# Optimization experiments

Measured on AMD Instinct MI355X. Metric: run time of the kernel, lower is better.

## Reference

```python
import jax, jax.numpy as jnp
import numpy as np
import math

D_MODEL = 512
NHEAD = 8
HEAD = D_MODEL // NHEAD


def _pe(length, d):
    pos = np.arange(length)[:, None].astype(np.float32)
    div = np.exp(np.arange(0, d, 2).astype(np.float32) * (-math.log(10000.0) / d))
    pe = np.zeros((length, d), np.float32)
    pe[:, 0::2] = np.sin(pos * div)
    pe[:, 1::2] = np.cos(pos * div)
    return jnp.asarray(pe)


def _ln(x, g, b, eps=1e-5):
    m = x.mean(-1, keepdims=True)
    v = ((x - m) ** 2).mean(-1, keepdims=True)
    return (x - m) / jnp.sqrt(v + eps) * g + b


def _mha(q_in, k_in, v_in, w_in, b_in, w_out, b_out, mask=None):
    d = q_in.shape[-1]
    wq, wk, wv = jnp.split(w_in, 3, axis=0)
    bq, bk, bv = jnp.split(b_in, 3, axis=0)
    B, Sq, _ = q_in.shape
    Sk = k_in.shape[1]
    q = (q_in @ wq.T + bq).reshape(B, Sq, NHEAD, HEAD)
    k = (k_in @ wk.T + bk).reshape(B, Sk, NHEAD, HEAD)
    v = (v_in @ wv.T + bv).reshape(B, Sk, NHEAD, HEAD)
    s = jnp.einsum('bqhd,bkhd->bhqk', q, k) / math.sqrt(HEAD)
    if mask is not None:
        s = s + mask
    a = jax.nn.softmax(s, axis=-1)
    o = jnp.einsum('bhqk,bkhd->bqhd', a, v).reshape(B, Sq, d)
    return o @ w_out.T + b_out


def setup_inputs() -> dict:
    rng = np.random.default_rng(0)
    def r(*s):
        return jnp.asarray(rng.standard_normal(s, dtype=np.float32) * 0.02)
    L, d, ff, di, do = 6, 512, 2048, 64, 64
    B, S, T = 4, 512, 256
    return dict(
        src=jnp.asarray(rng.standard_normal((B, S, di), dtype=np.float32)),
        tgt=jnp.asarray(rng.standard_normal((B, T, do), dtype=np.float32)),
        enc_in_w=r(d, di), enc_in_b=r(d),
        dec_in_w=r(d, do), dec_in_b=r(d),
        out_w=r(do, d), out_b=r(do),
        enc_attn_w=r(L, 3 * d, d), enc_attn_b=r(L, 3 * d),
        enc_out_w=r(L, d, d), enc_out_b=r(L, d),
        enc_ff1_w=r(L, ff, d), enc_ff1_b=r(L, ff),
        enc_ff2_w=r(L, d, ff), enc_ff2_b=r(L, d),
        enc_ln1_g=jnp.ones((L, d)), enc_ln1_b=jnp.zeros((L, d)),
        enc_ln2_g=jnp.ones((L, d)), enc_ln2_b=jnp.zeros((L, d)),
        dec_sa_w=r(L, 3 * d, d), dec_sa_b=r(L, 3 * d),
        dec_sa_out_w=r(L, d, d), dec_sa_out_b=r(L, d),
        dec_ca_w=r(L, 3 * d, d), dec_ca_b=r(L, 3 * d),
        dec_ca_out_w=r(L, d, d), dec_ca_out_b=r(L, d),
        dec_ff1_w=r(L, ff, d), dec_ff1_b=r(L, ff),
        dec_ff2_w=r(L, d, ff), dec_ff2_b=r(L, d),
        dec_ln1_g=jnp.ones((L, d)), dec_ln1_b=jnp.zeros((L, d)),
        dec_ln2_g=jnp.ones((L, d)), dec_ln2_b=jnp.zeros((L, d)),
        dec_ln3_g=jnp.ones((L, d)), dec_ln3_b=jnp.zeros((L, d)),
    )


def reference(src, tgt, enc_in_w, enc_in_b, dec_in_w, dec_in_b, out_w, out_b,
              enc_attn_w, enc_attn_b, enc_out_w, enc_out_b,
              enc_ff1_w, enc_ff1_b, enc_ff2_w, enc_ff2_b,
              enc_ln1_g, enc_ln1_b, enc_ln2_g, enc_ln2_b,
              dec_sa_w, dec_sa_b, dec_sa_out_w, dec_sa_out_b,
              dec_ca_w, dec_ca_b, dec_ca_out_w, dec_ca_out_b,
              dec_ff1_w, dec_ff1_b, dec_ff2_w, dec_ff2_b,
              dec_ln1_g, dec_ln1_b, dec_ln2_g, dec_ln2_b, dec_ln3_g, dec_ln3_b):
    d = D_MODEL
    sq = math.sqrt(d)
    S, T = src.shape[1], tgt.shape[1]
    L = enc_attn_w.shape[0]
    # encoder: 'cosine' pos encoding (dropout disabled / eval)
    x = (src @ enc_in_w.T + enc_in_b) * sq + _pe(S, d)[None]
    for i in range(L):
        a = _mha(x, x, x, enc_attn_w[i], enc_attn_b[i], enc_out_w[i], enc_out_b[i])
        x = _ln(x + a, enc_ln1_g[i], enc_ln1_b[i])
        f = jax.nn.relu(x @ enc_ff1_w[i].T + enc_ff1_b[i]) @ enc_ff2_w[i].T + enc_ff2_b[i]
        x = _ln(x + f, enc_ln2_g[i], enc_ln2_b[i])
    memory = x
    # decoder: teacher-forced prefix loop == single causal-masked pass.
    # NOTE: original adds pe[0] to EVERY step (pos_encoder on a length-1 slice).
    y = (tgt @ dec_in_w.T + dec_in_b) * sq + _pe(1, d)[0]
    mask = jnp.where(jnp.tril(jnp.ones((T, T), bool)), 0.0, -1e9).astype(y.dtype)
    for i in range(L):
        a = _mha(y, y, y, dec_sa_w[i], dec_sa_b[i], dec_sa_out_w[i], dec_sa_out_b[i], mask)
        y = _ln(y + a, dec_ln1_g[i], dec_ln1_b[i])
        c = _mha(y, memory, memory, dec_ca_w[i], dec_ca_b[i], dec_ca_out_w[i], dec_ca_out_b[i])
        y = _ln(y + c, dec_ln2_g[i], dec_ln2_b[i])
        f = jax.nn.relu(y @ dec_ff1_w[i].T + dec_ff1_b[i]) @ dec_ff2_w[i].T + dec_ff2_b[i]
        y = _ln(y + f, dec_ln3_g[i], dec_ln3_b[i])
    return y @ out_w.T + out_b
```

## Files before the change

### kernel.cpp

```cpp
#include <hip/hip_runtime.h>
#include <hip/hip_bf16.h>
#include <math.h>

#define BB 4
#define SEQ 512
#define TGT 256
#define DM 512
#define FFD 2048
#define NH 8
#define HD 64
#define NL 6

typedef unsigned short u16;
typedef __attribute__((ext_vector_type(4))) float f4;
typedef __attribute__((ext_vector_type(4))) unsigned short us4;
typedef __attribute__((ext_vector_type(8))) unsigned short us8;
typedef __attribute__((ext_vector_type(8))) short s8;

__device__ inline u16 f2b(float f) {
    __hip_bfloat16 h = __float2bfloat16(f);
    return *reinterpret_cast<u16*>(&h);
}
__device__ inline float b2f(u16 u) {
    unsigned int x = ((unsigned int)u) << 16;
    float f;
    __builtin_memcpy(&f, &x, 4);
    return f;
}
__device__ inline us4 cvt4(f4 v) {
    us4 u;
    u.x = f2b(v.x); u.y = f2b(v.y); u.z = f2b(v.z); u.w = f2b(v.w);
    return u;
}

struct CastSegs {
    const float* src[24];
    u16* dst[24];
    int cum[25];
    int nseg;
};

__global__ __launch_bounds__(256) void castseg_k(CastSegs cs)
{
    int i = blockIdx.x * blockDim.x + threadIdx.x;
    if (i >= cs.cum[cs.nseg]) return;
    int s = 0;
    while (i >= cs.cum[s + 1]) s++;
    int local = i - cs.cum[s];
    const f4* sp = (const f4*)cs.src[s] + (size_t)local * 2;
    f4 lo = sp[0], hi = sp[1];
    us4 ul = cvt4(lo), uh = cvt4(hi);
    us8 o;
#pragma unroll
    for (int e = 0; e < 4; e++) { o[e] = ul[e]; o[e + 4] = uh[e]; }
    ((us8*)cs.dst[s])[local] = o;
}

__global__ void kvbias_k(const float* __restrict__ dec_ca_b, float* __restrict__ out)
{
    int idx = blockIdx.x * blockDim.x + threadIdx.x;
    if (idx >= NL * 2 * DM) return;
    int layer = idx >> 10, j = idx & 1023;
    out[idx] = dec_ca_b[layer * 3 * DM + DM + j];
}

template <int RELU, int OUTF32, int BM, int PE>
__global__ __launch_bounds__(256) void mgemm_k(
    const u16* __restrict__ A, const u16* __restrict__ W,
    const float* __restrict__ bias, const u16* __restrict__ resid,
    void* __restrict__ Cv, int M, int N, int K, float alpha)
{
    constexpr int MI = BM / 32;
    __shared__ u16 As[2][BM][72];
    __shared__ u16 Bs[2][64][72];
    const int bm = blockIdx.y * BM, bn = blockIdx.x * 64;
    const int tid = threadIdx.x;
    const int wave = tid >> 6, lane = tid & 63;
    const int wr = (wave >> 1) * (BM / 2), wc = (wave & 1) * 32;
    const int lm = lane & 15, quad = lane >> 4;
    const int sbr = tid >> 2, sbc = (tid & 3) * 16;
    const int sar = (BM == 64) ? (tid >> 2) : (tid >> 3);
    const int sac = (BM == 64) ? ((tid & 3) * 16) : ((tid & 7) * 8);

    const u16* Arow = A + (size_t)(bm + sar) * K + sac;
    const u16* Wrow = W + (size_t)(bn + sbr) * K + sbc;

    us8 a0 = *(const us8*)(Arow);
    us8 a1;
    if (BM == 64) a1 = *(const us8*)(Arow + 8);
    us8 b0 = *(const us8*)(Wrow);
    us8 b1 = *(const us8*)(Wrow + 8);

    f4 acc[MI][2];
#pragma unroll
    for (int i = 0; i < MI; i++)
#pragma unroll
        for (int j = 0; j < 2; j++) acc[i][j] = (f4)(0.f);

    const int nk = K >> 6;
    *(us8*)&As[0][sar][sac] = a0;
    if (BM == 64) *(us8*)&As[0][sar][sac + 8] = a1;
    *(us8*)&Bs[0][sbr][sbc] = b0;
    *(us8*)&Bs[0][sbr][sbc + 8] = b1;
    __syncthreads();

    for (int t = 0; t < nk; t++) {
        const int cb = t & 1;
        if (t + 1 < nk) {
            int off = (t + 1) << 6;
            a0 = *(const us8*)(Arow + off);
            if (BM == 64) a1 = *(const us8*)(Arow + off + 8);
            b0 = *(const us8*)(Wrow + off);
            b1 = *(const us8*)(Wrow + off + 8);
        }
#pragma unroll
        for (int ks = 0; ks < 2; ks++) {
            s8 af[MI], bfr[2];
#pragma unroll
            for (int i = 0; i < MI; i++) af[i] = *(const s8*)&As[cb][wr + i * 16 + lm][ks * 32 + quad * 8];
#pragma unroll
            for (int j = 0; j < 2; j++) bfr[j] = *(const s8*)&Bs[cb][wc + j * 16 + lm][ks * 32 + quad * 8];
#pragma unroll
            for (int i = 0; i < MI; i++)
#pragma unroll
                for (int j = 0; j < 2; j++)
                    acc[i][j] = __builtin_amdgcn_mfma_f32_16x16x32_bf16(af[i], bfr[j], acc[i][j], 0, 0, 0);
        }
        if (t + 1 < nk) {
            const int nb = cb ^ 1;
            *(us8*)&As[nb][sar][sac] = a0;
            if (BM == 64) *(us8*)&As[nb][sar][sac + 8] = a1;
            *(us8*)&Bs[nb][sbr][sbc] = b0;
            *(us8*)&Bs[nb][sbr][sbc + 8] = b1;
            __syncthreads();
        }
    }

#pragma unroll
    for (int j = 0; j < 2; j++) {
        int n = bn + wc + j * 16 + lm;
        float bv = bias[n];
        float dv = 0.f;
        if (PE == 1) dv = expf((float)(n & ~1) * (-9.210340371976184f / (float)DM));
#pragma unroll
        for (int i = 0; i < MI; i++) {
#pragma unroll
            for (int r = 0; r < 4; r++) {
                int m = bm + wr + i * 16 + quad * 4 + r;
                float v = (acc[i][j][r] + bv) * alpha;
                if (PE == 1) {
                    float ang = (float)(m & (SEQ - 1)) * dv;
                    v += (n & 1) ? cosf(ang) : sinf(ang);
                }
                if (PE == 2) { if (n & 1) v += 1.f; }
                if (RELU) v = fmaxf(v, 0.f);
                size_t off = (size_t)m * N + n;
                if (resid) v += b2f(resid[off]);
                if (OUTF32) ((float*)Cv)[off] = v;
                else        ((u16*)Cv)[off]  = f2b(v);
            }
        }
    }
}

template <int RELU>
__global__ __launch_bounds__(256) void mgemm128_k(
    const u16* __restrict__ A, const u16* __restrict__ W,
    const float* __restrict__ bias, u16* __restrict__ C,
    int M, int N, int K)
{
    __shared__ u16 As[2][64][72];
    __shared__ u16 Bs[2][128][72];
    const int bm = blockIdx.y * 64, bn = blockIdx.x * 128;
    const int tid = threadIdx.x;
    const int wave = tid >> 6, lane = tid & 63;
    const int wr = (wave >> 1) * 32, wc = (wave & 1) * 64;
    const int lm = lane & 15, quad = lane >> 4;
    const int sar = tid >> 2, sac = (tid & 3) * 16;
    const int sbr = tid >> 1, sbc = (tid & 1) * 32;

    const u16* Arow = A + (size_t)(bm + sar) * K + sac;
    const u16* Wrow = W + (size_t)(bn + sbr) * K + sbc;

    us8 a0 = *(const us8*)(Arow);
    us8 a1 = *(const us8*)(Arow + 8);
    us8 b0 = *(const us8*)(Wrow);
    us8 b1 = *(const us8*)(Wrow + 8);
    us8 b2 = *(const us8*)(Wrow + 16);
    us8 b3 = *(const us8*)(Wrow + 24);

    f4 acc[2][4];
#pragma unroll
    for (int i = 0; i < 2; i++)
#pragma unroll
        for (int j = 0; j < 4; j++) acc[i][j] = (f4)(0.f);

    const int nk = K >> 6;
    *(us8*)&As[0][sar][sac]     = a0;
    *(us8*)&As[0][sar][sac + 8] = a1;
    *(us8*)&Bs[0][sbr][sbc]      = b0;
    *(us8*)&Bs[0][sbr][sbc + 8]  = b1;
    *(us8*)&Bs[0][sbr][sbc + 16] = b2;
    *(us8*)&Bs[0][sbr][sbc + 24] = b3;
    __syncthreads();

    for (int t = 0; t < nk; t++) {
        const int cb = t & 1;
        if (t + 1 < nk) {
            int off = (t + 1) << 6;
            a0 = *(const us8*)(Arow + off);
            a1 = *(const us8*)(Arow + off + 8);
            b0 = *(const us8*)(Wrow + off);
            b1 = *(const us8*)(Wrow + off + 8);
            b2 = *(const us8*)(Wrow + off + 16);
            b3 = *(const us8*)(Wrow + off + 24);
        }
#pragma unroll
        for (int ks = 0; ks < 2; ks++) {
            s8 af[2], bfr[4];
#pragma unroll
            for (int i = 0; i < 2; i++) af[i] = *(const s8*)&As[cb][wr + i * 16 + lm][ks * 32 + quad * 8];
#pragma unroll
            for (int j = 0; j < 4; j++) bfr[j] = *(const s8*)&Bs[cb][wc + j * 16 + lm][ks * 32 + quad * 8];
#pragma unroll
            for (int i = 0; i < 2; i++)
#pragma unroll
                for (int j = 0; j < 4; j++)
                    acc[i][j] = __builtin_amdgcn_mfma_f32_16x16x32_bf16(af[i], bfr[j], acc[i][j], 0, 0, 0);
        }
        if (t + 1 < nk) {
            const int nb = cb ^ 1;
            *(us8*)&As[nb][sar][sac]     = a0;
            *(us8*)&As[nb][sar][sac + 8] = a1;
            *(us8*)&Bs[nb][sbr][sbc]      = b0;
            *(us8*)&Bs[nb][sbr][sbc + 8]  = b1;
            *(us8*)&Bs[nb][sbr][sbc + 16] = b2;
            *(us8*)&Bs[nb][sbr][sbc + 24] = b3;
            __syncthreads();
        }
    }

#pragma unroll
    for (int j = 0; j < 4; j++) {
        int n = bn + wc + j * 16 + lm;
        float bv = bias[n];
#pragma unroll
        for (int i = 0; i < 2; i++) {
#pragma unroll
            for (int r = 0; r < 4; r++) {
                int m = bm + wr + i * 16 + quad * 4 + r;
                float v = acc[i][j][r] + bv;
                if (RELU) v = fmaxf(v, 0.f);
                C[(size_t)m * N + n] = f2b(v);
            }
        }
    }
}

template <int CAUSAL>
__global__ __launch_bounds__(256) void flash_k(
    const u16* __restrict__ Q, int qs,
    const u16* __restrict__ Kp, int ks,
    const u16* __restrict__ V, int vs,
    u16* __restrict__ O, int Sq, int Sk)
{
    __shared__ u16 Qs[64][72];
    __shared__ u16 Ks[128][72];
    __shared__ u16 Vs[64][136];
    __shared__ u16 Ps[4][16][136];
    const int bm = blockIdx.x * 64;
    const int bh = blockIdx.y, b = bh >> 3, h = bh & 7;
    const int tid = threadIdx.x;
    const int wave = tid >> 6, lane = tid & 63;
    const int lm = lane & 15, quad = lane >> 4;

    const u16* Qb = Q + (size_t)(b * Sq + bm) * qs + h * HD;
    {
        int r = tid >> 2, c = (tid & 3) * 16;
        *(us8*)&Qs[r][c]     = *(const us8*)(Qb + (size_t)r * qs + c);
        *(us8*)&Qs[r][c + 8] = *(const us8*)(Qb + (size_t)r * qs + c + 8);
    }

    float mrow[4], lrow[4];
    f4 o[4];
#pragma unroll
    for (int r = 0; r < 4; r++) { mrow[r] = -1e30f; lrow[r] = 0.f; }
#pragma unroll
    for (int nt = 0; nt < 4; nt++) o[nt] = (f4)(0.f);

    const u16* Kb = Kp + (size_t)(b * Sk) * ks + h * HD;
    const u16* Vb = V + (size_t)(b * Sk) * vs + h * HD;
    int nkt = Sk >> 7;
    if (CAUSAL) { int lim = (bm + 63) / 128 + 1; if (lim < nkt) nkt = lim; }

    const int vd = tid & 63, vkb = tid >> 6;
    const int kr = tid >> 3, kc8 = (tid & 7) * 8;

    for (int kt = 0; kt < nkt; kt++) {
        const u16* Kt = Kb + ((size_t)kt << 7) * ks;
        const u16* Vt = Vb + ((size_t)kt << 7) * vs;
#pragma unroll
        for (int p = 0; p < 4; p++) {
            int r = p * 32 + kr;
            *(us8*)&Ks[r][kc8] = *(const us8*)(Kt + (size_t)r * ks + kc8);
        }
#pragma unroll
        for (int p = 0; p < 32; p++) {
            int kv = p * 4 + vkb;
            Vs[vd][kv] = Vt[(size_t)kv * vs + vd];
        }
        __syncthreads();

        f4 sa[8];
#pragma unroll
        for (int nt = 0; nt < 8; nt++) sa[nt] = (f4)(0.f);
#pragma unroll
        for (int ks2 = 0; ks2 < 2; ks2++) {
            s8 aq = *(const s8*)&Qs[wave * 16 + lm][ks2 * 32 + quad * 8];
#pragma unroll
            for (int nt = 0; nt < 8; nt++) {
                s8 bk = *(const s8*)&Ks[nt * 16 + lm][ks2 * 32 + quad * 8];
                sa[nt] = __builtin_amdgcn_mfma_f32_16x16x32_bf16(aq, bk, sa[nt], 0, 0, 0);
            }
        }
        float tmx[4] = {-1e30f, -1e30f, -1e30f, -1e30f};
#pragma unroll
        for (int nt = 0; nt < 8; nt++) {
#pragma unroll
            for (int r = 0; r < 4; r++) {
                float v = sa[nt][r] * 0.125f;
                if (CAUSAL) {
                    int col = (kt << 7) + nt * 16 + lm;
                    int row = bm + wave * 16 + quad * 4 + r;
                    if (col > row) v = -1e30f;
                }
                sa[nt][r] = v;
                tmx[r] = fmaxf(tmx[r], v);
            }
        }
#pragma unroll
        for (int st = 1; st < 16; st <<= 1)
#pragma unroll
            for (int r = 0; r < 4; r++) tmx[r] = fmaxf(tmx[r], __shfl_xor(tmx[r], st));
        float al[4];
#pragma unroll
        for (int r = 0; r < 4; r++) {
            float mn = fmaxf(mrow[r], tmx[r]);
            al[r] = __expf(mrow[r] - mn);
            mrow[r] = mn;
        }
        float ts[4] = {0.f, 0.f, 0.f, 0.f};
#pragma unroll
        for (int nt = 0; nt < 8; nt++) {
#pragma unroll
            for (int r = 0; r < 4; r++) {
                float pe = __expf(sa[nt][r] - mrow[r]);
                sa[nt][r] = pe;
                ts[r] += pe;
            }
        }
#pragma unroll
        for (int st = 1; st < 16; st <<= 1)
#pragma unroll
            for (int r = 0; r < 4; r++) ts[r] += __shfl_xor(ts[r], st);
#pragma unroll
        for (int r = 0; r < 4; r++) lrow[r] = lrow[r] * al[r] + ts[r];
#pragma unroll
        for (int nt = 0; nt < 4; nt++)
#pragma unroll
            for (int r = 0; r < 4; r++) o[nt][r] *= al[r];
#pragma unroll
        for (int nt = 0; nt < 8; nt++)
#pragma unroll
            for (int r = 0; r < 4; r++)
                Ps[wave][quad * 4 + r][nt * 16 + lm] = f2b(sa[nt][r]);
#pragma unroll
        for (int kc = 0; kc < 4; kc++) {
            s8 ap = *(const s8*)&Ps[wave][lm][kc * 32 + quad * 8];
#pragma unroll
            for (int nt = 0; nt < 4; nt++) {
                s8 bv = *(const s8*)&Vs[nt * 16 + lm][kc * 32 + quad * 8];
                o[nt] = __builtin_amdgcn_mfma_f32_16x16x32_bf16(ap, bv, o[nt], 0, 0, 0);
            }
        }
        __syncthreads();
    }

    float inv[4];
#pragma unroll
    for (int r = 0; r < 4; r++) inv[r] = 1.f / lrow[r];
#pragma unroll
    for (int nt = 0; nt < 4; nt++) {
#pragma unroll
        for (int r = 0; r < 4; r++) {
            int m = bm + wave * 16 + quad * 4 + r;
            O[(size_t)(b * Sq + m) * DM + h * HD + nt * 16 + lm] = f2b(o[nt][r] * inv[r]);
        }
    }
}

__global__ __launch_bounds__(256) void ln_k(u16* __restrict__ x,
                                            const float* __restrict__ g,
                                            const float* __restrict__ b)
{
    const int wave = threadIdx.x >> 6, lane = threadIdx.x & 63;
    const int row = blockIdx.x * 4 + wave;
    u16* xr = x + (size_t)row * DM + lane * 8;
    us8 v8 = *(const us8*)xr;
    float v[8];
    float s = 0.f;
#pragma unroll
    for (int e = 0; e < 8; e++) { v[e] = b2f(v8[e]); s += v[e]; }
#pragma unroll
    for (int st = 1; st < 64; st <<= 1) s += __shfl_xor(s, st);
    float mean = s * (1.f / DM);
    float q = 0.f;
#pragma unroll
    for (int e = 0; e < 8; e++) { float d = v[e] - mean; q += d * d; }
#pragma unroll
    for (int st = 1; st < 64; st <<= 1) q += __shfl_xor(q, st);
    float rstd = rsqrtf(q * (1.f / DM) + 1e-5f);
    f4 g0 = *(const f4*)(g + lane * 8), g1 = *(const f4*)(g + lane * 8 + 4);
    f4 b0 = *(const f4*)(b + lane * 8), b1 = *(const f4*)(b + lane * 8 + 4);
    us8 o;
#pragma unroll
    for (int e = 0; e < 4; e++) {
        o[e]     = f2b((v[e]     - mean) * rstd * g0[e] + b0[e]);
        o[e + 4] = f2b((v[e + 4] - mean) * rstd * g1[e] + b1[e]);
    }
    *(us8*)xr = o;
}

static inline dim3 mg64(int M, int N) { return dim3(N / 64, M / 64); }
static inline dim3 mg32(int M, int N) { return dim3(N / 64, M / 32); }
static inline dim3 mg128(int M, int N) { return dim3(N / 128, M / 64); }

extern "C" void kernel_launch(void* const* d_in, const int* in_sizes, int n_in,
                              void* d_out, int out_size, void* d_ws, size_t ws_size,
                              hipStream_t stream)
{
    const float* src       = (const float*)d_in[0];
    const float* tgt       = (const float*)d_in[1];
    const float* enc_in_w  = (const float*)d_in[2];
    const float* enc_in_b  = (const float*)d_in[3];
    const float* dec_in_w  = (const float*)d_in[4];
    const float* dec_in_b  = (const float*)d_in[5];
    const float* out_w     = (const float*)d_in[6];
    const float* out_b     = (const float*)d_in[7];
    const float* enc_attn_w = (const float*)d_in[8];
    const float* enc_attn_b = (const float*)d_in[9];
    const float* enc_out_w  = (const float*)d_in[10];
    const float* enc_out_b  = (const float*)d_in[11];
    const float* enc_ff1_w  = (const float*)d_in[12];
    const float* enc_ff1_b  = (const float*)d_in[13];
    const float* enc_ff2_w  = (const float*)d_in[14];
    const float* enc_ff2_b  = (const float*)d_in[15];
    const float* enc_ln1_g  = (const float*)d_in[16];
    const float* enc_ln1_b  = (const float*)d_in[17];
    const float* enc_ln2_g  = (const float*)d_in[18];
    const float* enc_ln2_b  = (const float*)d_in[19];
    const float* dec_sa_w     = (const float*)d_in[20];
    const float* dec_sa_b     = (const float*)d_in[21];
    const float* dec_sa_out_w = (const float*)d_in[22];
    const float* dec_sa_out_b = (const float*)d_in[23];
    const float* dec_ca_w     = (const float*)d_in[24];
    const float* dec_ca_b     = (const float*)d_in[25];
    const float* dec_ca_out_w = (const float*)d_in[26];
    const float* dec_ca_out_b = (const float*)d_in[27];
    const float* dec_ff1_w    = (const float*)d_in[28];
    const float* dec_ff1_b    = (const float*)d_in[29];
    const float* dec_ff2_w    = (const float*)d_in[30];
    const float* dec_ff2_b    = (const float*)d_in[31];
    const float* dec_ln1_g    = (const float*)d_in[32];
    const float* dec_ln1_b    = (const float*)d_in[33];
    const float* dec_ln2_g    = (const float*)d_in[34];
    const float* dec_ln2_b    = (const float*)d_in[35];
    const float* dec_ln3_g    = (const float*)d_in[36];
    const float* dec_ln3_b    = (const float*)d_in[37];

    const int ME = BB * SEQ;
    const int MD = BB * TGT;
    const int BH = BB * NH;
    const float SQD = 22.627416997969522f;

    const size_t SZ_ATTN = (size_t)NL * 3 * DM * DM;
    const size_t SZ_OUT  = (size_t)NL * DM * DM;
    const size_t SZ_FF   = (size_t)NL * FFD * DM;

    float* fp = (float*)d_ws;
    float* kvbias = fp; fp += NL * 2 * DM;
    u16* p = (u16*)fp;
    u16* xa   = p; p += (size_t)ME * DM;
    u16* xb   = p; p += (size_t)ME * DM;
    u16* reg1 = p; p += (size_t)ME * FFD;
    u16* tbuf = p; p += (size_t)ME * DM;
    u16* ya   = p; p += (size_t)MD * DM;
    u16* yb   = p; p += (size_t)MD * DM;
    u16* kvall = p; p += (size_t)ME * NL * 2 * DM;
    u16* src_b     = p; p += (size_t)ME * HD;
    u16* tgt_b     = p; p += (size_t)MD * HD;
    u16* enc_in_wb = p; p += (size_t)DM * HD;
    u16* dec_in_wb = p; p += (size_t)DM * HD;
    u16* out_wb    = p; p += (size_t)HD * DM;
    u16* enc_at_wb = p; p += SZ_ATTN;
    u16* enc_ow_wb = p; p += SZ_OUT;
    u16* enc_f1_wb = p; p += SZ_FF;
    u16* enc_f2_wb = p; p += SZ_FF;
    u16* dec_sa_wb = p; p += SZ_ATTN;
    u16* dec_sao_wb = p; p += SZ_OUT;
    u16* dec_ca_wb = p; p += SZ_ATTN;
    u16* dec_cao_wb = p; p += SZ_OUT;
    u16* dec_f1_wb = p; p += SZ_FF;
    u16* dec_f2_wb = p; p += SZ_FF;
    u16* kvstack   = p; p += (size_t)NL * 2 * DM * DM;

    CastSegs cs;
    int ns = 0;
    auto seg = [&](const float* s, u16* d, size_t n) {
        cs.src[ns] = s; cs.dst[ns] = d;
        cs.cum[ns + 1] = cs.cum[ns] + (int)(n / 8);
        ns++;
    };
    cs.cum[0] = 0;
    seg(src,          src_b,     (size_t)ME * HD);
    seg(tgt,          tgt_b,     (size_t)MD * HD);
    seg(enc_in_w,     enc_in_wb, (size_t)DM * HD);
    seg(dec_in_w,     dec_in_wb, (size_t)DM * HD);
    seg(out_w,        out_wb,    (size_t)HD * DM);
    seg(enc_attn_w,   enc_at_wb, SZ_ATTN);
    seg(enc_out_w,    enc_ow_wb, SZ_OUT);
    seg(enc_ff1_w,    enc_f1_wb, SZ_FF);
    seg(enc_ff2_w,    enc_f2_wb, SZ_FF);
    seg(dec_sa_w,     dec_sa_wb, SZ_ATTN);
    seg(dec_sa_out_w, dec_sao_wb, SZ_OUT);
    seg(dec_ca_w,     dec_ca_wb, SZ_ATTN);
    seg(dec_ca_out_w, dec_cao_wb, SZ_OUT);
    seg(dec_ff1_w,    dec_f1_wb, SZ_FF);
    seg(dec_ff2_w,    dec_f2_wb, SZ_FF);
    for (int i = 0; i < NL; i++)
        seg(dec_ca_w + (size_t)i * 3 * DM * DM + (size_t)DM * DM,
            kvstack + (size_t)i * 2 * DM * DM, (size_t)2 * DM * DM);
    cs.nseg = ns;
    castseg_k<<<(cs.cum[ns] + 255) / 256, 256, 0, stream>>>(cs);
    kvbias_k<<<(NL * 2 * DM + 255) / 256, 256, 0, stream>>>(dec_ca_b, kvbias);

    mgemm_k<0, 0, 64, 1><<<mg64(ME, DM), 256, 0, stream>>>(src_b, enc_in_wb, enc_in_b, nullptr, xa, ME, DM, HD, SQD);

    u16* cur = xa; u16* alt = xb;
    for (int i = 0; i < NL; i++) {
        const u16* W = enc_at_wb + (size_t)i * 3 * DM * DM;
        const float* Bw = enc_attn_b + (size_t)i * 3 * DM;
        mgemm128_k<0><<<mg128(ME, 3 * DM), 256, 0, stream>>>(cur, W, Bw, reg1, ME, 3 * DM, DM);
        flash_k<0><<<dim3(SEQ / 64, BH), 256, 0, stream>>>(reg1, 3 * DM, reg1 + DM, 3 * DM, reg1 + 2 * DM, 3 * DM, tbuf, SEQ, SEQ);
        mgemm_k<0, 0, 32, 0><<<mg32(ME, DM), 256, 0, stream>>>(tbuf, enc_ow_wb + (size_t)i * DM * DM, enc_out_b + (size_t)i * DM, cur, alt, ME, DM, DM, 1.f);
        ln_k<<<ME / 4, 256, 0, stream>>>(alt, enc_ln1_g + (size_t)i * DM, enc_ln1_b + (size_t)i * DM);
        { u16* t = cur; cur = alt; alt = t; }
        mgemm128_k<1><<<mg128(ME, FFD), 256, 0, stream>>>(cur, enc_f1_wb + (size_t)i * FFD * DM, enc_ff1_b + (size_t)i * FFD, reg1, ME, FFD, DM);
        mgemm_k<0, 0, 32, 0><<<mg32(ME, DM), 256, 0, stream>>>(reg1, enc_f2_wb + (size_t)i * DM * FFD, enc_ff2_b + (size_t)i * DM, cur, alt, ME, DM, FFD, 1.f);
        ln_k<<<ME / 4, 256, 0, stream>>>(alt, enc_ln2_g + (size_t)i * DM, enc_ln2_b + (size_t)i * DM);
        { u16* t = cur; cur = alt; alt = t; }
    }
    u16* mem = cur;

    mgemm128_k<0><<<mg128(ME, NL * 2 * DM), 256, 0, stream>>>(mem, kvstack, kvbias, kvall, ME, NL * 2 * DM, DM);

    mgemm_k<0, 0, 32, 2><<<mg32(MD, DM), 256, 0, stream>>>(tgt_b, dec_in_wb, dec_in_b, nullptr, ya, MD, DM, HD, SQD);

    u16* dc = ya; u16* da = yb;
    for (int i = 0; i < NL; i++) {
        const u16* W = dec_sa_wb + (size_t)i * 3 * DM * DM;
        const float* Bw = dec_sa_b + (size_t)i * 3 * DM;
        mgemm128_k<0><<<mg128(MD, 3 * DM), 256, 0, stream>>>(dc, W, Bw, reg1, MD, 3 * DM, DM);
        flash_k<1><<<dim3(TGT / 64, BH), 256, 0, stream>>>(reg1, 3 * DM, reg1 + DM, 3 * DM, reg1 + 2 * DM, 3 * DM, tbuf, TGT, TGT);
        mgemm_k<0, 0, 32, 0><<<mg32(MD, DM), 256, 0, stream>>>(tbuf, dec_sao_wb + (size_t)i * DM * DM, dec_sa_out_b + (size_t)i * DM, dc, da, MD, DM, DM, 1.f);
        ln_k<<<MD / 4, 256, 0, stream>>>(da, dec_ln1_g + (size_t)i * DM, dec_ln1_b + (size_t)i * DM);
        { u16* t = dc; dc = da; da = t; }

        const u16* Wc = dec_ca_wb + (size_t)i * 3 * DM * DM;
        const float* Bc = dec_ca_b + (size_t)i * 3 * DM;
        u16* qbuf = reg1;
        mgemm_k<0, 0, 32, 0><<<mg32(MD, DM), 256, 0, stream>>>(dc, Wc, Bc, nullptr, qbuf, MD, DM, DM, 1.f);
        const u16* kvl = kvall + (size_t)i * 2 * DM;
        flash_k<0><<<dim3(TGT / 64, BH), 256, 0, stream>>>(qbuf, DM, kvl, NL * 2 * DM, kvl + DM, NL * 2 * DM, tbuf, TGT, SEQ);
        mgemm_k<0, 0, 32, 0><<<mg32(MD, DM), 256, 0, stream>>>(tbuf, dec_cao_wb + (size_t)i * DM * DM, dec_ca_out_b + (size_t)i * DM, dc, da, MD, DM, DM, 1.f);
        ln_k<<<MD / 4, 256, 0, stream>>>(da, dec_ln2_g + (size_t)i * DM, dec_ln2_b + (size_t)i * DM);
        { u16* t = dc; dc = da; da = t; }

        mgemm128_k<1><<<mg128(MD, FFD), 256, 0, stream>>>(dc, dec_f1_wb + (size_t)i * FFD * DM, dec_ff1_b + (size_t)i * FFD, reg1, MD, FFD, DM);
        mgemm_k<0, 0, 32, 0><<<mg32(MD, DM), 256, 0, stream>>>(reg1, dec_f2_wb + (size_t)i * DM * FFD, dec_ff2_b + (size_t)i * DM, dc, da, MD, DM, FFD, 1.f);
        ln_k<<<MD / 4, 256, 0, stream>>>(da, dec_ln3_g + (size_t)i * DM, dec_ln3_b + (size_t)i * DM);
        { u16* t = dc; dc = da; da = t; }
    }

    mgemm_k<0, 1, 32, 0><<<mg32(MD, HD), 256, 0, stream>>>(dc, out_wb, out_b, nullptr, (float*)d_out, MD, HD, DM, 1.f);
}
```

Baseline: 1.258 ms.

## Stage GEMM tiles via direct global-to-LDS loads with XOR-swizzled layout

```diff
diff --git a/kernel.cpp b/kernel.cpp
--- a/kernel.cpp
+++ b/kernel.cpp
@@ -31,6 +31,13 @@
     us4 u;
     u.x = f2b(v.x); u.y = f2b(v.y); u.z = f2b(v.z); u.w = f2b(v.w);
     return u;
+}
+
+__device__ inline void load_lds16(const u16* g, u16* l) {
+    __builtin_amdgcn_global_load_lds(
+        (const __attribute__((address_space(1))) void*)g,
+        (__attribute__((address_space(3))) void*)l,
+        16, 0, 0);
 }
 
 struct CastSegs {
@@ -71,25 +78,18 @@
     void* __restrict__ Cv, int M, int N, int K, float alpha)
 {
     constexpr int MI = BM / 32;
-    __shared__ u16 As[2][BM][72];
-    __shared__ u16 Bs[2][64][72];
+    __shared__ __align__(16) u16 As[2][BM][64];
+    __shared__ __align__(16) u16 Bs[2][64][64];
     const int bm = blockIdx.y * BM, bn = blockIdx.x * 64;
     const int tid = threadIdx.x;
     const int wave = tid >> 6, lane = tid & 63;
     const int wr = (wave >> 1) * (BM / 2), wc = (wave & 1) * 32;
     const int lm = lane & 15, quad = lane >> 4;
-    const int sbr = tid >> 2, sbc = (tid & 3) * 16;
-    const int sar = (BM == 64) ? (tid >> 2) : (tid >> 3);
-    const int sac = (BM == 64) ? ((tid & 3) * 16) : ((tid & 7) * 8);
-
-    const u16* Arow = A + (size_t)(bm + sar) * K + sac;
-    const u16* Wrow = W + (size_t)(bn + sbr) * K + sbc;
-
-    us8 a0 = *(const us8*)(Arow);
-    us8 a1;
-    if (BM == 64) a1 = *(const us8*)(Arow + 8);
-    us8 b0 = *(const us8*)(Wrow);
-    us8 b1 = *(const us8*)(Wrow + 8);
+
+    const int srow = lane >> 3;
+    const int scol = (((lane & 7) ^ srow) * 8);
+
+    const int nk = K >> 6;
 
     f4 acc[MI][2];
 #pragma unroll
@@ -97,43 +97,38 @@
 #pragma unroll
         for (int j = 0; j < 2; j++) acc[i][j] = (f4)(0.f);
 
-    const int nk = K >> 6;
-    *(us8*)&As[0][sar][sac] = a0;
-    if (BM == 64) *(us8*)&As[0][sar][sac + 8] = a1;
-    *(us8*)&Bs[0][sbr][sbc] = b0;
-    *(us8*)&Bs[0][sbr][sbc + 8] = b1;
+    auto stage = [&](int buf, int t) {
+        const int koff = t << 6;
+#pragma unroll
+        for (int g = wave; g < BM / 8; g += 4)
+            load_lds16(A + (size_t)(bm + g * 8 + srow) * K + koff + scol, &As[buf][g * 8][0]);
+#pragma unroll
+        for (int g = wave; g < 8; g += 4)
+            load_lds16(W + (size_t)(bn + g * 8 + srow) * K + koff + scol, &Bs[buf][g * 8][0]);
+    };
+
+    stage(0, 0);
     __syncthreads();
 
+    const int xb = lm & 7;
     for (int t = 0; t < nk; t++) {
         const int cb = t & 1;
-        if (t + 1 < nk) {
-            int off = (t + 1) << 6;
-            a0 = *(const us8*)(Arow + off);
-            if (BM == 64) a1 = *(const us8*)(Arow + off + 8);
-            b0 = *(const us8*)(Wrow + off);
-            b1 = *(const us8*)(Wrow + off + 8);
-        }
+        if (t + 1 < nk) stage(cb ^ 1, t + 1);
 #pragma unroll
         for (int ks = 0; ks < 2; ks++) {
+            const int xs = ((ks * 4 + quad) ^ xb) * 8;
             s8 af[MI], bfr[2];
 #pragma unroll
-            for (int i = 0; i < MI; i++) af[i] = *(const s8*)&As[cb][wr + i * 16 + lm][ks * 32 + quad * 8];
-#pragma unroll
-            for (int j = 0; j < 2; j++) bfr[j] = *(const s8*)&Bs[cb][wc + j * 16 + lm][ks * 32 + quad * 8];
+            for (int i = 0; i < MI; i++) af[i] = *(const s8*)&As[cb][wr + i * 16 + lm][xs];
+#pragma unroll
+            for (int j = 0; j < 2; j++) bfr[j] = *(const s8*)&Bs[cb][wc + j * 16 + lm][xs];
 #pragma unroll
             for (int i = 0; i < MI; i++)
 #pragma unroll
                 for (int j = 0; j < 2; j++)
                     acc[i][j] = __builtin_amdgcn_mfma_f32_16x16x32_bf16(af[i], bfr[j], acc[i][j], 0, 0, 0);
         }
-        if (t + 1 < nk) {
-            const int nb = cb ^ 1;
-            *(us8*)&As[nb][sar][sac] = a0;
-            if (BM == 64) *(us8*)&As[nb][sar][sac + 8] = a1;
-            *(us8*)&Bs[nb][sbr][sbc] = b0;
-            *(us8*)&Bs[nb][sbr][sbc + 8] = b1;
-            __syncthreads();
-        }
+        if (t + 1 < nk) __syncthreads();
     }
 
 #pragma unroll
@@ -169,25 +164,18 @@
     const float* __restrict__ bias, u16* __restrict__ C,
     int M, int N, int K)
 {
-    __shared__ u16 As[2][64][72];
-    __shared__ u16 Bs[2][128][72];
+    __shared__ __align__(16) u16 As[2][64][64];
+    __shared__ __align__(16) u16 Bs[2][128][64];
     const int bm = blockIdx.y * 64, bn = blockIdx.x * 128;
     const int tid = threadIdx.x;
     const int wave = tid >> 6, lane = tid & 63;
     const int wr = (wave >> 1) * 32, wc = (wave & 1) * 64;
     const int lm = lane & 15, quad = lane >> 4;
-    const int sar = tid >> 2, sac = (tid & 3) * 16;
-    const int sbr = tid >> 1, sbc = (tid & 1) * 32;
-
-    const u16* Arow = A + (size_t)(bm + sar) * K + sac;
-    const u16* Wrow = W + (size_t)(bn + sbr) * K + sbc;
-
-    us8 a0 = *(const us8*)(Arow);
-    us8 a1 = *(const us8*)(Arow + 8);
-    us8 b0 = *(const us8*)(Wrow);
-    us8 b1 = *(const us8*)(Wrow + 8);
-    us8 b2 = *(const us8*)(Wrow + 16);
-    us8 b3 = *(const us8*)(Wrow + 24);
+
+    const int srow = lane >> 3;
+    const int scol = (((lane & 7) ^ srow) * 8);
+
+    const int nk = K >> 6;
 
     f4 acc[2][4];
 #pragma unroll
@@ -195,49 +183,38 @@
 #pragma unroll
         for (int j = 0; j < 4; j++) acc[i][j] = (f4)(0.f);
 
-    const int nk = K >> 6;
-    *(us8*)&As[0][sar][sac]     = a0;
-    *(us8*)&As[0][sar][sac + 8] = a1;
-    *(us8*)&Bs[0][sbr][sbc]      = b0;
-    *(us8*)&Bs[0][sbr][sbc + 8]  = b1;
-    *(us8*)&Bs[0][sbr][sbc + 16] = b2;
-    *(us8*)&Bs[0][sbr][sbc + 24] = b3;
+    auto stage = [&](int buf, int t) {
+        const int koff = t << 6;
+#pragma unroll
+        for (int g = wave; g < 8; g += 4)
+            load_lds16(A + (size_t)(bm + g * 8 + srow) * K + koff + scol, &As[buf][g * 8][0]);
+#pragma unroll
+        for (int g = wave; g < 16; g += 4)
+            load_lds16(W + (size_t)(bn + g * 8 + srow) * K + koff + scol, &Bs[buf][g * 8][0]);
+    };
+
+    stage(0, 0);
     __syncthreads();
 
+    const int xb = lm & 7;
     for (int t = 0; t < nk; t++) {
         const int cb = t & 1;
-        if (t + 1 < nk) {
-            int off = (t + 1) << 6;
-            a0 = *(const us8*)(Arow + off);
-            a1 = *(const us8*)(Arow + off + 8);
-            b0 = *(const us8*)(Wrow + off);
-            b1 = *(const us8*)(Wrow + off + 8);
-            b2 = *(const us8*)(Wrow + off + 16);
-            b3 = *(const us8*)(Wrow + off + 24);
-        }
+        if (t + 1 < nk) stage(cb ^ 1, t + 1);
 #pragma unroll
         for (int ks = 0; ks < 2; ks++) {
+            const int xs = ((ks * 4 + quad) ^ xb) * 8;
             s8 af[2], bfr[4];
 #pragma unroll
-            for (int i = 0; i < 2; i++) af[i] = *(const s8*)&As[cb][wr + i * 16 + lm][ks * 32 + quad * 8];
-#pragma unroll
-            for (int j = 0; j < 4; j++) bfr[j] = *(const s8*)&Bs[cb][wc + j * 16 + lm][ks * 32 + quad * 8];
+            for (int i = 0; i < 2; i++) af[i] = *(const s8*)&As[cb][wr + i * 16 + lm][xs];
+#pragma unroll
+            for (int j = 0; j < 4; j++) bfr[j] = *(const s8*)&Bs[cb][wc + j * 16 + lm][xs];
 #pragma unroll
             for (int i = 0; i < 2; i++)
 #pragma unroll
                 for (int j = 0; j < 4; j++)
                     acc[i][j] = __builtin_amdgcn_mfma_f32_16x16x32_bf16(af[i], bfr[j], acc[i][j], 0, 0, 0);
         }
-        if (t + 1 < nk) {
-            const int nb = cb ^ 1;
-            *(us8*)&As[nb][sar][sac]     = a0;
-            *(us8*)&As[nb][sar][sac + 8] = a1;
-            *(us8*)&Bs[nb][sbr][sbc]      = b0;
-            *(us8*)&Bs[nb][sbr][sbc + 8]  = b1;
-            *(us8*)&Bs[nb][sbr][sbc + 16] = b2;
-            *(us8*)&Bs[nb][sbr][sbc + 24] = b3;
-            __syncthreads();
-        }
+        if (t + 1 < nk) __syncthreads();
     }
 
 #pragma unroll
```

Result: slower. 1.327 ms (+5.5%).
